# Kernel tuning notes

Hardware: AMD Instinct MI355X
Metric: run time of the kernel (lower is better)

The kernel has to match this reference:

```python
import jax, jax.numpy as jnp
import numpy as np

SCALE = 2      # shuffle_scale
K = 3          # nearest neighbors / conv kernel size (stride == K)
SAMPLES = 16   # sample grid size per axis -> M = SAMPLES**2


def pixel_unshuffle(x, s):
    B, C, H, W = x.shape
    x = x.reshape(B, C, H // s, s, W // s, s)
    x = x.transpose(0, 1, 3, 5, 2, 4)
    return x.reshape(B, C * s * s, H // s, W // s)


def pixel_shuffle(x, s):
    B, C, H, W = x.shape
    x = x.reshape(B, C // (s * s), s, s, H, W)
    x = x.transpose(0, 1, 4, 2, 5, 3)
    return x.reshape(B, C // (s * s), H * s, W * s)


def setup_inputs() -> dict:
    key = jax.random.key(0)
    k1, k2, k3 = jax.random.split(key, 3)
    x = jax.random.normal(k1, (32, 16, 128, 128), dtype=jnp.float32)
    weight = jax.random.normal(k2, (64, 64, K), dtype=jnp.float32) * 0.05  # [out_1d, in_1d, K]
    bias = jax.random.normal(k3, (64,), dtype=jnp.float32) * 0.05
    return {"x": x, "weight": weight, "bias": bias}


def reference(x, weight, bias):
    # --- pixel unshuffle ('B' part of 'BA') ---
    x1 = pixel_unshuffle(x, SCALE)                 # [B, C1=64, H1=64, W1=64]
    B, C1, H1, W1 = x1.shape
    N = H1 * W1

    # --- spatial subsample grid (linspace + round, sample_padding=0) ---
    xi = jnp.round(jnp.linspace(0.0, H1 - 1.0, SAMPLES)).astype(jnp.int32)
    yi = jnp.round(jnp.linspace(0.0, W1 - 1.0, SAMPLES)).astype(jnp.int32)
    xg, yg = jnp.meshgrid(xi, yi, indexing="ij")
    x_sample = x1[:, :, xg, yg].reshape(B, C1, -1)  # [B, C1, M]
    x2 = x1.reshape(B, C1, N)                       # [B, C1, N]

    # --- pairwise squared euclidean distance tokens -> samples ---
    # (sqrt omitted: monotone; top-k uses only indices, matching torch topk(largest=False))
    n2 = jnp.sum(x2 * x2, axis=1)                   # [B, N]
    m2 = jnp.sum(x_sample * x_sample, axis=1)       # [B, M]
    dot = jnp.einsum("bcn,bcm->bnm", x2, x_sample)  # [B, N, M]
    d2 = n2[:, :, None] + m2[:, None, :] - 2.0 * dot

    # --- K nearest sampled points per token ---
    _, idx = jax.lax.top_k(-d2, K)                  # [B, N, K]

    # --- gather neighbor features ('prime'); equals x2 at flat_indices[idx] ---
    prime = jnp.take_along_axis(x_sample[:, :, None, :], idx[:, None, :, :], axis=3)  # [B, C1, N, K]

    # --- Conv1d(kernel=K, stride=K) over [B, C1, N*K] == per-token contraction ---
    out = jnp.einsum("bcnk,ock->bon", prime, weight) + bias[None, :, None]  # [B, O1=64, N]
    out = out.reshape(B, weight.shape[0], H1, W1)

    # --- pixel shuffle ('A' part of 'BA') ---
    return pixel_shuffle(out, SCALE)                # [B, 16, 128, 128]
```

## Files before the change

kernel.cpp:

```cpp
#include <hip/hip_runtime.h>
#include <cstdint>
#include <cfloat>

typedef float v2f __attribute__((ext_vector_type(2)));

__constant__ int c_smp[16] = {0,4,8,13,17,21,25,29,34,38,42,46,50,55,59,63};

static constexpr int NB   = 32;
static constexpr int NC   = 64;
static constexpr int NH   = 64;
static constexpr int NTOK = 4096;
static constexpr int NM   = 256;
static constexpr int NK   = 3;

__global__ __launch_bounds__(256) void k_pre(const float* __restrict__ x,
                                             const float* __restrict__ w,
                                             float* __restrict__ wT,
                                             float* __restrict__ xs_t) {
    __shared__ __align__(16) float rows[16][2][128];
    if (blockIdx.x >= NB * 16) {
        int f = (blockIdx.x - NB * 16) * 256 + threadIdx.x;
        float v = w[f];
        int o = f / 192, rem = f % 192;
        int c = rem / 3, k = rem % 3;
        wT[((size_t)k * 64 + c) * 64 + o] = v;
        return;
    }
    int b = blockIdx.x >> 4, gi = blockIdx.x & 15;
    int hh = c_smp[gi];
    int t = threadIdx.x;
    const float* xb = x + (size_t)b * 16 * 128 * 128;
#pragma unroll
    for (int it = 0; it < 4; ++it) {
        int q = t + it * 256;
        int c = q >> 6;
        int rem = q & 63;
        int sh = rem >> 5;
        int col = (rem & 31) * 4;
        float4 v = *(const float4*)(xb + ((size_t)c * 128 + (2 * hh + sh)) * 128 + col);
        *(float4*)&rows[c][sh][col] = v;
    }
    __syncthreads();
    {
        int c1 = t >> 2;
        int c = c1 >> 2, sh = (c1 >> 1) & 1, sw = c1 & 1;
        int gj0 = (t & 3) * 4;
        float4 v;
        v.x = rows[c][sh][2 * c_smp[gj0 + 0] + sw];
        v.y = rows[c][sh][2 * c_smp[gj0 + 1] + sw];
        v.z = rows[c][sh][2 * c_smp[gj0 + 2] + sw];
        v.w = rows[c][sh][2 * c_smp[gj0 + 3] + sw];
        *(float4*)&xs_t[((size_t)b * NC + c1) * NM + gi * 16 + gj0] = v;
    }
}

__global__ __launch_bounds__(256) void k_z2(const float* __restrict__ xs_t,
                                            const float* __restrict__ wT,
                                            float* __restrict__ Z) {
    __shared__ __align__(16) float wL[64][64];
    __shared__ __align__(16) float xt[16][64];
    int bid = blockIdx.x;
    int mq = bid & 3;
    int k  = (bid >> 2) % 3;
    int b  = bid / 12;
    int t  = threadIdx.x;
    int mg = t >> 4, og = t & 15;

#pragma unroll
    for (int it = 0; it < 4; ++it) {
        int q = t + it * 256;
        int c = q >> 4;
        int o4 = (q & 15) * 4;
        *(float4*)&wL[c][o4] = *(const float4*)&wT[(size_t)k * 4096 + q * 4];
    }

    v2f acc[4][2];
#pragma unroll
    for (int i = 0; i < 4; ++i) { acc[i][0] = (v2f)(0.f); acc[i][1] = (v2f)(0.f); }

    for (int cc = 0; cc < 4; ++cc) {
        __syncthreads();
        {
            int c = t >> 4, m4 = (t & 15) * 4;
            *(float4*)&xt[c][m4] =
                *(const float4*)&xs_t[((size_t)b * NC + cc * 16 + c) * NM + mq * 64 + m4];
        }
        __syncthreads();
#pragma unroll
        for (int c = 0; c < 16; ++c) {
            float4 a4 = *(const float4*)&xt[c][mg * 4];
            float4 b4 = *(const float4*)&wL[cc * 16 + c][og * 4];
            v2f bp0 = {b4.x, b4.y}, bp1 = {b4.z, b4.w};
            float aa[4] = {a4.x, a4.y, a4.z, a4.w};
#pragma unroll
            for (int i = 0; i < 4; ++i) {
                v2f ai = {aa[i], aa[i]};
                acc[i][0] = __builtin_elementwise_fma(ai, bp0, acc[i][0]);
                acc[i][1] = __builtin_elementwise_fma(ai, bp1, acc[i][1]);
            }
        }
    }

    float* zb = Z + (((size_t)b * 3 + k) * NM + mq * 64) * NC;
#pragma unroll
    for (int i = 0; i < 4; ++i) {
        int m = mg * 4 + i;
        float4 v = {acc[i][0][0], acc[i][0][1], acc[i][1][0], acc[i][1][1]};
        *(float4*)&zb[(size_t)m * NC + og * 4] = v;
    }
}

static __device__ __forceinline__ unsigned long long packkey(float d, int m) {
    unsigned u = __float_as_uint(d);
    u ^= ((unsigned)((int)u >> 31)) | 0x80000000u;
    return ((unsigned long long)u << 32) | (unsigned)m;
}

__global__ __launch_bounds__(256) void k_dist(const float* __restrict__ x,
                                              const float* __restrict__ xs_t,
                                              int* __restrict__ idx) {
    __shared__ __align__(16) float att[16][64];
    __shared__ __align__(16) float xsB[16][256];
    __shared__ __align__(16) float m2l[256];
    __shared__ __align__(16) float n2l[64];

    int b = blockIdx.x >> 6;
    int h = blockIdx.x & 63;
    int t = threadIdx.x;
    int r = t >> 4, cl = t & 15;

    v2f acc2[4][8];
#pragma unroll
    for (int i = 0; i < 4; ++i)
#pragma unroll
        for (int j = 0; j < 8; ++j) acc2[i][j] = (v2f)(0.f);

    float m2acc = 0.f, n2acc = 0.f;
    const float* xb = x + (size_t)b * 16 * 128 * 128;
    const float* xsb = xs_t + (size_t)b * NC * NM;

    for (int kc = 0; kc < 4; ++kc) {
        __syncthreads();
#pragma unroll
        for (int it = 0; it < 2; ++it) {
            int i = t + it * 256;
            int p = i >> 6;
            int wcol = i & 63;
            int c1e = kc * 16 + p * 2;
            int c = c1e >> 2, sh = (c1e >> 1) & 1;
            const float* src = xb + ((size_t)c * 128 + (2 * h + sh)) * 128 + 2 * wcol;
            float2 v = *(const float2*)src;
            att[p * 2 + 0][wcol] = v.x;
            att[p * 2 + 1][wcol] = v.y;
        }
#pragma unroll
        for (int it = 0; it < 4; ++it) {
            int g = t + it * 256;
            int row = g >> 6;
            int m4 = g & 63;
            int dst = ((((m4 & 3) << 4) | (m4 >> 2))) << 2;
            *(float4*)&xsB[row][dst] =
                *(const float4*)&xsb[(size_t)(kc * 16 + row) * NM + m4 * 4];
        }
        __syncthreads();

#pragma unroll
        for (int c = 0; c < 16; ++c) {
            float v = xsB[c][t];
            m2acc = __fadd_rn(m2acc, __fmul_rn(v, v));
        }
        if (t < 64) {
#pragma unroll
            for (int c = 0; c < 16; ++c) {
                float v = att[c][t];
                n2acc = __fadd_rn(n2acc, __fmul_rn(v, v));
            }
        }

#pragma unroll
        for (int k = 0; k < 16; ++k) {
            float4 a0 = *(const float4*)&att[k][r * 4];
            float4 b0 = *(const float4*)&xsB[k][(0 * 16 + cl) * 4];
            float4 b1 = *(const float4*)&xsB[k][(1 * 16 + cl) * 4];
            float4 b2 = *(const float4*)&xsB[k][(2 * 16 + cl) * 4];
            float4 b3 = *(const float4*)&xsB[k][(3 * 16 + cl) * 4];
            v2f bp0 = {b0.x, b0.y}, bp1 = {b0.z, b0.w};
            v2f bp2 = {b1.x, b1.y}, bp3 = {b1.z, b1.w};
            v2f bp4 = {b2.x, b2.y}, bp5 = {b2.z, b2.w};
            v2f bp6 = {b3.x, b3.y}, bp7 = {b3.z, b3.w};
            float aa[4] = {a0.x, a0.y, a0.z, a0.w};
#pragma unroll
            for (int i = 0; i < 4; ++i) {
                v2f ai = {aa[i], aa[i]};
                acc2[i][0] = __builtin_elementwise_fma(ai, bp0, acc2[i][0]);
                acc2[i][1] = __builtin_elementwise_fma(ai, bp1, acc2[i][1]);
                acc2[i][2] = __builtin_elementwise_fma(ai, bp2, acc2[i][2]);
                acc2[i][3] = __builtin_elementwise_fma(ai, bp3, acc2[i][3]);
                acc2[i][4] = __builtin_elementwise_fma(ai, bp4, acc2[i][4]);
                acc2[i][5] = __builtin_elementwise_fma(ai, bp5, acc2[i][5]);
                acc2[i][6] = __builtin_elementwise_fma(ai, bp6, acc2[i][6]);
                acc2[i][7] = __builtin_elementwise_fma(ai, bp7, acc2[i][7]);
            }
        }
    }

    m2l[((t >> 2) & 15) * 16 + (t >> 6) * 4 + (t & 3)] = m2acc;
    if (t < 64) n2l[t] = n2acc;
    __syncthreads();

    float m2r[16];
#pragma unroll
    for (int j = 0; j < 16; ++j) m2r[j] = m2l[cl * 16 + j];

#pragma unroll
    for (int i = 0; i < 4; ++i) {
        int nloc = r * 4 + i;
        float n2v = n2l[nloc];
        float e0d = FLT_MAX, e1d = FLT_MAX, e2d = FLT_MAX;
        int e0m = 0x7fffffff, e1m = 0x7fffffff, e2m = 0x7fffffff;
#pragma unroll
        for (int j = 0; j < 16; ++j) {
            float dv = acc2[i][j >> 1][j & 1];
            float t1 = __fadd_rn(n2v, m2r[j]);
            float d = __fadd_rn(t1, -2.0f * dv);
            int m = cl * 16 + j;
            if (d < e2d) {
                e2d = d; e2m = m;
                if (e2d < e1d) {
                    float td = e1d; int tm = e1m; e1d = e2d; e1m = e2m;
                    e2d = td; e2m = tm;
                    if (e1d < e0d) {
                        float sd = e0d; int sm = e0m; e0d = e1d; e0m = e1m;
                        e1d = sd; e1m = sm;
                    }
                }
            }
        }
        unsigned long long k0 = packkey(e0d, e0m);
        unsigned long long k1 = packkey(e1d, e1m);
        unsigned long long k2 = packkey(e2d, e2m);
#pragma unroll
        for (int mask = 1; mask <= 8; mask <<= 1) {
            unsigned long long q0 = __shfl_xor(k0, mask);
            unsigned long long q1 = __shfl_xor(k1, mask);
            unsigned long long q2 = __shfl_xor(k2, mask);
            unsigned long long clo = k0 < q0 ? k0 : q0;
            unsigned long long chi = k0 < q0 ? q0 : k0;
            unsigned long long dlo = k1 < q1 ? k1 : q1;
            unsigned long long dhi = k1 < q1 ? q1 : k1;
            unsigned long long f2  = k2 < q2 ? k2 : q2;
            unsigned long long elo = chi < dlo ? chi : dlo;
            unsigned long long ehi = chi < dlo ? dlo : chi;
            unsigned long long g2  = dhi < f2 ? dhi : f2;
            k0 = clo;
            k1 = elo;
            k2 = ehi < g2 ? ehi : g2;
        }
        if (cl == 0) {
            int n = h * 64 + nloc;
            int* op = idx + ((size_t)b * NTOK + n) * NK;
            op[0] = (int)(unsigned)(k0 & 0xffffffffu);
            op[1] = (int)(unsigned)(k1 & 0xffffffffu);
            op[2] = (int)(unsigned)(k2 & 0xffffffffu);
        }
    }
}

__global__ __launch_bounds__(256) void k_out(const float* __restrict__ Z,
                                             const int* __restrict__ idx,
                                             const float* __restrict__ bias,
                                             float* __restrict__ out) {
    __shared__ float staged[64 * 65];
    int b = blockIdx.x >> 6, h = blockIdx.x & 63;
    int t = threadIdx.x;
    int o = t & 63, wv = t >> 6;
    float bv = bias[o];
    const float* zb = Z + (size_t)b * 3 * NM * NC;
    const int* ib = idx + (size_t)b * NTOK * NK;
    for (int ti = 0; ti < 16; ++ti) {
        int w = wv * 16 + ti;
        int n = h * 64 + w;
        const int* ip = ib + (size_t)n * NK;
        int i0 = ip[0], i1 = ip[1], i2 = ip[2];
        float v = bv + zb[(size_t)i0 * NC + o]
                     + zb[(size_t)(NM + i1) * NC + o]
                     + zb[(size_t)(2 * NM + i2) * NC + o];
        staged[o * 65 + w] = v;
    }
    __syncthreads();
    float* ob = out + (size_t)b * 16 * 128 * 128;
#pragma unroll
    for (int it = 0; it < 16; ++it) {
        int flat = t + it * 256;
        int W = flat & 127, sh = (flat >> 7) & 1, cc = flat >> 8;
        int oo = cc * 4 + sh * 2 + (W & 1);
        ob[((size_t)cc * 128 + 2 * h + sh) * 128 + W] = staged[oo * 65 + (W >> 1)];
    }
}

extern "C" void kernel_launch(void* const* d_in, const int* in_sizes, int n_in,
                              void* d_out, int out_size, void* d_ws, size_t ws_size,
                              hipStream_t stream) {
    const float* x    = (const float*)d_in[0];
    const float* w    = (const float*)d_in[1];
    const float* bias = (const float*)d_in[2];
    float* out = (float*)d_out;
    float* ws  = (float*)d_ws;

    float* xs_t = ws;
    float* Z    = ws + 524288;
    int*   idxb = (int*)(ws + 2097152);
    float* wT   = ws + 2490368;

    hipLaunchKernelGGL(k_pre,  dim3(NB * 16 + 48), dim3(256), 0, stream,
                       x, w, wT, xs_t);
    hipLaunchKernelGGL(k_z2,   dim3(NB * 3 * 4),   dim3(256), 0, stream,
                       xs_t, wT, Z);
    hipLaunchKernelGGL(k_dist, dim3(NB * 64),      dim3(256), 0, stream,
                       x, xs_t, idxb);
    hipLaunchKernelGGL(k_out,  dim3(NB * 64),      dim3(256), 0, stream,
                       Z, idxb, bias, out);
}
```

Baseline: 172.7 us.

## Fuse distance/top-k kernel with output gather kernel via shared-memory indices

Merges the k_dist and k_out kernels into one kernel, k_do. The top-3 neighbor indices per token now stay in shared memory instead of round-tripping through a global idx buffer. Shared memory is unioned so the staging tile reuses the distance buffers. This removes one kernel launch and the global write and read of indices. In exchange the fused kernel uses more registers and shared memory, which may lower occupancy.

```diff
diff --git a/kernel.cpp b/kernel.cpp
--- a/kernel.cpp
+++ b/kernel.cpp
@@ -116,13 +116,18 @@
     return ((unsigned long long)u << 32) | (unsigned)m;
 }
 
-__global__ __launch_bounds__(256) void k_dist(const float* __restrict__ x,
-                                              const float* __restrict__ xs_t,
-                                              int* __restrict__ idx) {
-    __shared__ __align__(16) float att[16][64];
-    __shared__ __align__(16) float xsB[16][256];
-    __shared__ __align__(16) float m2l[256];
-    __shared__ __align__(16) float n2l[64];
+__global__ __launch_bounds__(256) void k_do(const float* __restrict__ x,
+                                            const float* __restrict__ xs_t,
+                                            const float* __restrict__ Z,
+                                            const float* __restrict__ bias,
+                                            float* __restrict__ out) {
+    __shared__ __align__(16) float smem[5632];
+    float (*att)[64]  = (float(*)[64])smem;
+    float (*xsB)[256] = (float(*)[256])(smem + 1024);
+    float* m2l = smem + 5120;
+    float* n2l = smem + 5376;
+    int  (*idxL)[3] = (int(*)[3])(smem + 5440);
+    float* staged = smem;
 
     int b = blockIdx.x >> 6;
     int h = blockIdx.x & 63;
@@ -257,44 +262,34 @@
             k2 = ehi < g2 ? ehi : g2;
         }
         if (cl == 0) {
-            int n = h * 64 + nloc;
-            int* op = idx + ((size_t)b * NTOK + n) * NK;
-            op[0] = (int)(unsigned)(k0 & 0xffffffffu);
-            op[1] = (int)(unsigned)(k1 & 0xffffffffu);
-            op[2] = (int)(unsigned)(k2 & 0xffffffffu);
-        }
-    }
-}
-
-__global__ __launch_bounds__(256) void k_out(const float* __restrict__ Z,
-                                             const int* __restrict__ idx,
-                                             const float* __restrict__ bias,
-                                             float* __restrict__ out) {
-    __shared__ float staged[64 * 65];
-    int b = blockIdx.x >> 6, h = blockIdx.x & 63;
-    int t = threadIdx.x;
-    int o = t & 63, wv = t >> 6;
-    float bv = bias[o];
-    const float* zb = Z + (size_t)b * 3 * NM * NC;
-    const int* ib = idx + (size_t)b * NTOK * NK;
-    for (int ti = 0; ti < 16; ++ti) {
-        int w = wv * 16 + ti;
-        int n = h * 64 + w;
-        const int* ip = ib + (size_t)n * NK;
-        int i0 = ip[0], i1 = ip[1], i2 = ip[2];
-        float v = bv + zb[(size_t)i0 * NC + o]
-                     + zb[(size_t)(NM + i1) * NC + o]
-                     + zb[(size_t)(2 * NM + i2) * NC + o];
-        staged[o * 65 + w] = v;
+            idxL[nloc][0] = (int)(unsigned)(k0 & 0xffffffffu);
+            idxL[nloc][1] = (int)(unsigned)(k1 & 0xffffffffu);
+            idxL[nloc][2] = (int)(unsigned)(k2 & 0xffffffffu);
+        }
     }
     __syncthreads();
-    float* ob = out + (size_t)b * 16 * 128 * 128;
-#pragma unroll
-    for (int it = 0; it < 16; ++it) {
-        int flat = t + it * 256;
-        int W = flat & 127, sh = (flat >> 7) & 1, cc = flat >> 8;
-        int oo = cc * 4 + sh * 2 + (W & 1);
-        ob[((size_t)cc * 128 + 2 * h + sh) * 128 + W] = staged[oo * 65 + (W >> 1)];
+
+    {
+        int o = t & 63, wv = t >> 6;
+        float bv = bias[o];
+        const float* zb = Z + (size_t)b * 3 * NM * NC;
+        for (int ti = 0; ti < 16; ++ti) {
+            int w = wv * 16 + ti;
+            int i0 = idxL[w][0], i1 = idxL[w][1], i2 = idxL[w][2];
+            float v = bv + zb[(size_t)i0 * NC + o]
+                         + zb[(size_t)(NM + i1) * NC + o]
+                         + zb[(size_t)(2 * NM + i2) * NC + o];
+            staged[o * 65 + w] = v;
+        }
+        __syncthreads();
+        float* ob = out + (size_t)b * 16 * 128 * 128;
+#pragma unroll
+        for (int it = 0; it < 16; ++it) {
+            int flat = t + it * 256;
+            int W = flat & 127, sh = (flat >> 7) & 1, cc = flat >> 8;
+            int oo = cc * 4 + sh * 2 + (W & 1);
+            ob[((size_t)cc * 128 + 2 * h + sh) * 128 + W] = staged[oo * 65 + (W >> 1)];
+        }
     }
 }
 
@@ -309,15 +304,12 @@
 
     float* xs_t = ws;
     float* Z    = ws + 524288;
-    int*   idxb = (int*)(ws + 2097152);
-    float* wT   = ws + 2490368;
-
-    hipLaunchKernelGGL(k_pre,  dim3(NB * 16 + 48), dim3(256), 0, stream,
+    float* wT   = ws + 2097152;
+
+    hipLaunchKernelGGL(k_pre, dim3(NB * 16 + 48), dim3(256), 0, stream,
                        x, w, wT, xs_t);
-    hipLaunchKernelGGL(k_z2,   dim3(NB * 3 * 4),   dim3(256), 0, stream,
+    hipLaunchKernelGGL(k_z2,  dim3(NB * 3 * 4),   dim3(256), 0, stream,
                        xs_t, wT, Z);
-    hipLaunchKernelGGL(k_dist, dim3(NB * 64),      dim3(256), 0, stream,
-                       x, xs_t, idxb);
-    hipLaunchKernelGGL(k_out,  dim3(NB * 64),      dim3(256), 0, stream,
-                       Z, idxb, bias, out);
-}
+    hipLaunchKernelGGL(k_do,  dim3(NB * 64),      dim3(256), 0, stream,
+                       x, xs_t, Z, bias, out);
+}
```

After: 168.1 us (median of 3 runs). 1.03x faster.
